# Kernel tuning notes

Hardware: AMD Instinct MI355X
Metric: run time of the kernel (lower is better)

Reference implementation:

```python
import jax, jax.numpy as jnp
import numpy as np

LN_EPS = 1e-5
BN_EPS = 1e-5


def setup_inputs() -> dict:
    key = jax.random.key(0)
    ks = jax.random.split(key, 16)
    b, n = 16, 256
    sc = 0.1
    inp = {
        "x": jax.random.normal(ks[0], (b, n, 4), jnp.float32),
        # proj: Linear(4, 64)
        "proj_w": jax.random.normal(ks[1], (4, 64), jnp.float32) * sc,
        "proj_b": jnp.zeros((64,), jnp.float32),
        # sigma_net: Linear(128,64) -> LayerNorm(64) -> ReLU -> Linear(64,1) -> Softplus
        "s_w1": jax.random.normal(ks[2], (128, 64), jnp.float32) * sc,
        "s_b1": jnp.zeros((64,), jnp.float32),
        "ln_g": jnp.ones((64,), jnp.float32),
        "ln_b": jnp.zeros((64,), jnp.float32),
        "s_w2": jax.random.normal(ks[3], (64, 1), jnp.float32) * sc,
        "s_b2": jnp.zeros((1,), jnp.float32),
        # gnn weight
        "gnn_w": jax.random.normal(ks[4], (64, 64), jnp.float32) * sc,
        # classifier: Linear(128,64) -> BatchNorm1d(64) -> ELU -> Dropout(eval) -> Linear(64,2)
        "c_w1": jax.random.normal(ks[5], (128, 64), jnp.float32) * sc,
        "c_b1": jnp.zeros((64,), jnp.float32),
        "bn_g": jnp.ones((64,), jnp.float32),
        "bn_b": jnp.zeros((64,), jnp.float32),
        "bn_mean": jnp.zeros((64,), jnp.float32),
        "bn_var": jnp.ones((64,), jnp.float32),
        "c_w2": jax.random.normal(ks[6], (64, 2), jnp.float32) * sc,
        "c_b2": jnp.zeros((2,), jnp.float32),
    }
    return inp


def reference(x, proj_w, proj_b, s_w1, s_b1, ln_g, ln_b, s_w2, s_b2,
              gnn_w, c_w1, c_b1, bn_g, bn_b, bn_mean, bn_var, c_w2, c_b2):
    # h: [b, n, 64]
    h = jax.nn.elu(x @ proj_w + proj_b)

    # sigma_net(cat([xi, xj])) == hi @ s_w1[:64] + hj @ s_w1[64:] + s_b1, broadcast pairwise
    a_i = h @ s_w1[:64]            # [b, n, 64]
    a_j = h @ s_w1[64:]            # [b, n, 64]
    pre = a_i[:, :, None, :] + a_j[:, None, :, :] + s_b1  # [b, n, n, 64]
    mu = jnp.mean(pre, axis=-1, keepdims=True)
    var = jnp.mean((pre - mu) ** 2, axis=-1, keepdims=True)
    ln = (pre - mu) * jax.lax.rsqrt(var + LN_EPS) * ln_g + ln_b
    sig_pre = jax.nn.relu(ln) @ s_w2 + s_b2               # [b, n, n, 1]
    sigmas = jax.nn.softplus(sig_pre[..., 0])             # [b, n, n]

    # squared pairwise distance via gram trick: ||hi - hj||^2
    sq = jnp.sum(h * h, axis=-1)                          # [b, n]
    gram = jnp.einsum("bid,bjd->bij", h, h)               # [b, n, n]
    d2 = jnp.maximum(sq[:, :, None] + sq[:, None, :] - 2.0 * gram, 0.0)
    adj = jnp.exp(-d2 / (2.0 * sigmas ** 2 + 1e-6))       # [b, n, n]

    h_agg = jnp.einsum("bij,bjd->bid", adj, h) @ gnn_w    # [b, n, 64]
    h_res = jax.nn.elu(h_agg + h)

    pooled = jnp.concatenate([h_res.mean(axis=1), h_res.max(axis=1)], axis=1)  # [b, 128]

    z = pooled @ c_w1 + c_b1
    z = (z - bn_mean) * jax.lax.rsqrt(bn_var + BN_EPS) * bn_g + bn_b  # BN eval mode
    z = jax.nn.elu(z)                                      # Dropout is identity in eval
    return z @ c_w2 + c_b2                                 # [b, 2]
```

## Files before the change

### kernel.cpp

```cpp
#include <hip/hip_runtime.h>
#include <math.h>

#define OFF_H      0
#define OFF_HT     262144
#define OFF_AI     524288
#define OFF_AJT    786432
#define OFF_SAI    1048576
#define OFF_QAI    1052672
#define OFF_SAJ    1056768
#define OFF_QAJ    1060864
#define OFF_SQH    1064960
#define OFF_HRES   1069056

__device__ __forceinline__ float elu_f(float x) { return x > 0.f ? x : expm1f(x); }

__global__ __launch_bounds__(256) void k1_embed(
    const float* __restrict__ x,
    const float* __restrict__ proj_w, const float* __restrict__ proj_b,
    const float* __restrict__ s_w1, const float* __restrict__ s_b1,
    float* __restrict__ h, float* __restrict__ hT,
    float* __restrict__ a_i, float* __restrict__ a_jT,
    float* __restrict__ sa_i, float* __restrict__ qa_i,
    float* __restrict__ sa_j, float* __restrict__ qa_j,
    float* __restrict__ sqh)
{
    int lane = threadIdx.x & 63;
    int wave = threadIdx.x >> 6;
    int row  = blockIdx.x * 4 + wave;
    int b = row >> 8, i = row & 255;

    __shared__ float hsh[4][64];

    float4 xv = *(const float4*)&x[row*4];
    float hv = xv.x*proj_w[lane] + xv.y*proj_w[64+lane] + xv.z*proj_w[128+lane]
             + xv.w*proj_w[192+lane] + proj_b[lane];
    hv = elu_f(hv);
    hsh[wave][lane] = hv;
    __syncthreads();

    float ai = s_b1[lane], aj = 0.f;
    #pragma unroll 8
    for (int e = 0; e < 64; ++e) {
        float he = hsh[wave][e];
        ai = fmaf(he, s_w1[e*64 + lane], ai);
        aj = fmaf(he, s_w1[(64+e)*64 + lane], aj);
    }
    h[row*64 + lane] = hv;
    hT[b*64*256 + lane*256 + i] = hv;
    a_i[row*64 + lane] = ai;
    a_jT[b*64*256 + lane*256 + i] = aj;

    float v1 = ai, v2 = ai*ai, v3 = aj, v4 = aj*aj, v5 = hv*hv;
    #pragma unroll
    for (int off = 32; off > 0; off >>= 1) {
        v1 += __shfl_xor(v1, off);
        v2 += __shfl_xor(v2, off);
        v3 += __shfl_xor(v3, off);
        v4 += __shfl_xor(v4, off);
        v5 += __shfl_xor(v5, off);
    }
    if (lane == 0) {
        sa_i[row] = v1; qa_i[row] = v2;
        sa_j[row] = v3; qa_j[row] = v4;
        sqh[row]  = v5;
    }
}

#define TI 4
__global__ __launch_bounds__(256) void k2_pair(
    const float* __restrict__ a_i, const float* __restrict__ a_jT,
    const float* __restrict__ h, const float* __restrict__ hT,
    const float* __restrict__ sa_i, const float* __restrict__ qa_i,
    const float* __restrict__ sa_j, const float* __restrict__ qa_j,
    const float* __restrict__ sqh,
    const float* __restrict__ ln_g, const float* __restrict__ ln_b,
    const float* __restrict__ s_w2, const float* __restrict__ s_b2,
    const float* __restrict__ gnn_w,
    float* __restrict__ h_res)
{
    int bi0 = blockIdx.x * TI;
    int b   = bi0 >> 8;
    int j   = threadIdx.x;

    __shared__ float4 aj4[16][256];
    __shared__ float  aiT[64][4], hiT[64][4];
    __shared__ float  gbw[64][4];
    __shared__ float  sai_s[4], qai_s[4], sqi_s[4];
    __shared__ float  adj_sh[256][4];
    __shared__ float  part_sh[4][4][64];
    __shared__ float  hagg_sh[4][64];

    {
        int i = j >> 6, d = j & 63;
        aiT[d][i] = a_i[(bi0+i)*64 + d];
        hiT[d][i] = h[(bi0+i)*64 + d];
    }
    if (j < 64) {
        gbw[j][0] = ln_g[j]; gbw[j][1] = ln_b[j]; gbw[j][2] = s_w2[j]; gbw[j][3] = 0.f;
    }
    if (j < 4) {
        sai_s[j] = sa_i[bi0+j]; qai_s[j] = qa_i[bi0+j]; sqi_s[j] = sqh[bi0+j];
    }
    float saj = sa_j[b*256 + j], qaj = qa_j[b*256 + j], sqj = sqh[b*256 + j];
    float b2  = s_b2[0];
    __syncthreads();

    const float* ajb = a_jT + b*64*256;
    const float* htb = hT   + b*64*256;

    float ga[4] = {0.f,0.f,0.f,0.f}, gh[4] = {0.f,0.f,0.f,0.f};
    #pragma unroll 4
    for (int dg = 0; dg < 16; ++dg) {
        float c[4];
        #pragma unroll
        for (int u = 0; u < 4; ++u) {
            int d = dg*4 + u;
            float ajd = ajb[d*256 + j];
            float hjd = htb[d*256 + j];
            float4 A = *(const float4*)&aiT[d][0];
            float4 H = *(const float4*)&hiT[d][0];
            ga[0] = fmaf(A.x, ajd, ga[0]); ga[1] = fmaf(A.y, ajd, ga[1]);
            ga[2] = fmaf(A.z, ajd, ga[2]); ga[3] = fmaf(A.w, ajd, ga[3]);
            gh[0] = fmaf(H.x, hjd, gh[0]); gh[1] = fmaf(H.y, hjd, gh[1]);
            gh[2] = fmaf(H.z, hjd, gh[2]); gh[3] = fmaf(H.w, hjd, gh[3]);
            c[u] = ajd;
        }
        aj4[dg][j] = make_float4(c[0], c[1], c[2], c[3]);
    }

    float rs4[4], nr4[4], d24[4];
    #pragma unroll
    for (int i = 0; i < 4; ++i) {
        float mu  = (sai_s[i] + saj) * (1.f/64.f);
        float pss = qai_s[i] + qaj + 2.f*ga[i];
        float var = pss * (1.f/64.f) - mu*mu;
        rs4[i] = rsqrtf(var + 1e-5f);
        nr4[i] = -mu * rs4[i];
        d24[i] = fmaxf(sqi_s[i] + sqj - 2.f*gh[i], 0.f);
    }

    float acc[4] = {0.f,0.f,0.f,0.f};
    #pragma unroll 4
    for (int dg = 0; dg < 16; ++dg) {
        float4 ajv = aj4[dg][j];
        float aju[4] = {ajv.x, ajv.y, ajv.z, ajv.w};
        #pragma unroll
        for (int u = 0; u < 4; ++u) {
            int d = dg*4 + u;
            float ajd = aju[u];
            float4 A = *(const float4*)&aiT[d][0];
            float4 G = *(const float4*)&gbw[d][0];
            float t0 = fmaxf(fmaf(fmaf(A.x + ajd, rs4[0], nr4[0]), G.x, G.y), 0.f);
            acc[0] = fmaf(t0, G.z, acc[0]);
            float t1 = fmaxf(fmaf(fmaf(A.y + ajd, rs4[1], nr4[1]), G.x, G.y), 0.f);
            acc[1] = fmaf(t1, G.z, acc[1]);
            float t2 = fmaxf(fmaf(fmaf(A.z + ajd, rs4[2], nr4[2]), G.x, G.y), 0.f);
            acc[2] = fmaf(t2, G.z, acc[2]);
            float t3 = fmaxf(fmaf(fmaf(A.w + ajd, rs4[3], nr4[3]), G.x, G.y), 0.f);
            acc[3] = fmaf(t3, G.z, acc[3]);
        }
    }

    {
        float4 av;
        float sp0 = acc[0] + b2;
        float sg0 = fmaxf(sp0, 0.f) + log1pf(expf(-fabsf(sp0)));
        av.x = expf(-d24[0] / (2.f*sg0*sg0 + 1e-6f));
        float sp1 = acc[1] + b2;
        float sg1 = fmaxf(sp1, 0.f) + log1pf(expf(-fabsf(sp1)));
        av.y = expf(-d24[1] / (2.f*sg1*sg1 + 1e-6f));
        float sp2 = acc[2] + b2;
        float sg2 = fmaxf(sp2, 0.f) + log1pf(expf(-fabsf(sp2)));
        av.z = expf(-d24[2] / (2.f*sg2*sg2 + 1e-6f));
        float sp3 = acc[3] + b2;
        float sg3 = fmaxf(sp3, 0.f) + log1pf(expf(-fabsf(sp3)));
        av.w = expf(-d24[3] / (2.f*sg3*sg3 + 1e-6f));
        *(float4*)&adj_sh[j][0] = av;
    }
    __syncthreads();

    int d = j & 63, q = j >> 6;
    const float* hb = h + b*256*64;
    float part[4] = {0.f,0.f,0.f,0.f};
    #pragma unroll 8
    for (int k = 0; k < 64; ++k) {
        int jj = q*64 + k;
        float hv = hb[jj*64 + d];
        float4 a4 = *(const float4*)&adj_sh[jj][0];
        part[0] = fmaf(a4.x, hv, part[0]);
        part[1] = fmaf(a4.y, hv, part[1]);
        part[2] = fmaf(a4.z, hv, part[2]);
        part[3] = fmaf(a4.w, hv, part[3]);
    }
    #pragma unroll
    for (int i = 0; i < 4; ++i) part_sh[q][i][d] = part[i];
    __syncthreads();

    {
        int i = j >> 6, dd = j & 63;
        hagg_sh[i][dd] = part_sh[0][i][dd] + part_sh[1][i][dd]
                       + part_sh[2][i][dd] + part_sh[3][i][dd];
    }
    __syncthreads();

    {
        int i = j >> 6, lane = j & 63;
        float accg = 0.f;
        #pragma unroll 8
        for (int e = 0; e < 64; ++e)
            accg = fmaf(hagg_sh[i][e], gnn_w[e*64 + lane], accg);
        h_res[(bi0+i)*64 + lane] = elu_f(accg + hiT[lane][i]);
    }
}

__global__ __launch_bounds__(256) void k4_pool_cls(
    const float* __restrict__ h_res,
    const float* __restrict__ c_w1, const float* __restrict__ c_b1,
    const float* __restrict__ bn_g, const float* __restrict__ bn_b,
    const float* __restrict__ bn_mean, const float* __restrict__ bn_var,
    const float* __restrict__ c_w2, const float* __restrict__ c_b2,
    float* __restrict__ out)
{
    int b = blockIdx.x;
    int tid = threadIdx.x;
    int d = tid & 63, q = tid >> 6;
    const float* hb = h_res + b*256*64;

    float sum = 0.f, mx = -INFINITY;
    #pragma unroll 8
    for (int k = 0; k < 64; ++k) {
        float v = hb[(q*64+k)*64 + d];
        sum += v; mx = fmaxf(mx, v);
    }
    __shared__ float sum_sh[256], max_sh[256];
    __shared__ float pm_sh[64], px_sh[64];
    sum_sh[tid] = sum; max_sh[tid] = mx;
    __syncthreads();
    if (tid < 64) {
        float tsum = sum_sh[tid] + sum_sh[64+tid] + sum_sh[128+tid] + sum_sh[192+tid];
        float tmax = fmaxf(fmaxf(max_sh[tid], max_sh[64+tid]),
                           fmaxf(max_sh[128+tid], max_sh[192+tid]));
        pm_sh[tid] = tsum * (1.f/256.f);
        px_sh[tid] = tmax;
    }
    __syncthreads();
    if (tid < 64) {
        float acc = c_b1[tid];
        #pragma unroll
        for (int e = 0; e < 64; ++e) {
            acc += pm_sh[e] * c_w1[e*64 + tid];
            acc += px_sh[e] * c_w1[(64+e)*64 + tid];
        }
        float z = (acc - bn_mean[tid]) * rsqrtf(bn_var[tid] + 1e-5f) * bn_g[tid] + bn_b[tid];
        z = elu_f(z);
        float c0 = z * c_w2[tid*2 + 0];
        float c1 = z * c_w2[tid*2 + 1];
        for (int off = 32; off > 0; off >>= 1) {
            c0 += __shfl_down(c0, off);
            c1 += __shfl_down(c1, off);
        }
        if (tid == 0) {
            out[b*2 + 0] = c0 + c_b2[0];
            out[b*2 + 1] = c1 + c_b2[1];
        }
    }
}

extern "C" void kernel_launch(void* const* d_in, const int* in_sizes, int n_in,
                              void* d_out, int out_size, void* d_ws, size_t ws_size,
                              hipStream_t stream) {
    const float* x       = (const float*)d_in[0];
    const float* proj_w  = (const float*)d_in[1];
    const float* proj_b  = (const float*)d_in[2];
    const float* s_w1    = (const float*)d_in[3];
    const float* s_b1    = (const float*)d_in[4];
    const float* ln_g    = (const float*)d_in[5];
    const float* ln_b    = (const float*)d_in[6];
    const float* s_w2    = (const float*)d_in[7];
    const float* s_b2    = (const float*)d_in[8];
    const float* gnn_w   = (const float*)d_in[9];
    const float* c_w1    = (const float*)d_in[10];
    const float* c_b1    = (const float*)d_in[11];
    const float* bn_g    = (const float*)d_in[12];
    const float* bn_b    = (const float*)d_in[13];
    const float* bn_mean = (const float*)d_in[14];
    const float* bn_var  = (const float*)d_in[15];
    const float* c_w2    = (const float*)d_in[16];
    const float* c_b2    = (const float*)d_in[17];

    float* w = (float*)d_ws;
    float* h     = w + OFF_H;
    float* hT    = w + OFF_HT;
    float* a_i   = w + OFF_AI;
    float* a_jT  = w + OFF_AJT;
    float* sa_i  = w + OFF_SAI;
    float* qa_i  = w + OFF_QAI;
    float* sa_j  = w + OFF_SAJ;
    float* qa_j  = w + OFF_QAJ;
    float* sqh   = w + OFF_SQH;
    float* h_res = w + OFF_HRES;
    float* out   = (float*)d_out;

    k1_embed<<<1024, 256, 0, stream>>>(x, proj_w, proj_b, s_w1, s_b1,
                                       h, hT, a_i, a_jT,
                                       sa_i, qa_i, sa_j, qa_j, sqh);
    k2_pair<<<1024, 256, 0, stream>>>(a_i, a_jT, h, hT,
                                      sa_i, qa_i, sa_j, qa_j, sqh,
                                      ln_g, ln_b, s_w2, s_b2, gnn_w, h_res);
    k4_pool_cls<<<16, 256, 0, stream>>>(h_res, c_w1, c_b1, bn_g, bn_b,
                                        bn_mean, bn_var, c_w2, c_b2, out);
}
```

Baseline: 55.28 us.

## Drop transposed buffers, hold a_j rows in registers, stage s_w1 in LDS

The embed kernel now copies all of s_w1 into shared memory, has each wave process two rows, broadcasts h values with wave shuffles, and no longer writes transposed hT/a_jT. The pair kernel reads each j-row of h and a_j as row-major float4 vectors and keeps a_j in 16 float4 registers instead of a 16 KB shared-memory staging array, with launch bounds requesting 3 blocks per SM. This removes the strided transposed writes and the large LDS buffer, which should allow more blocks per CU. The cost is much higher register pressure, and each thread's row-major loads are 256 bytes apart from its neighbours' rather than coalesced across lanes.

```diff
diff --git a/kernel.cpp b/kernel.cpp
--- a/kernel.cpp
+++ b/kernel.cpp
@@ -2,15 +2,14 @@
 #include <math.h>
 
 #define OFF_H      0
-#define OFF_HT     262144
-#define OFF_AI     524288
-#define OFF_AJT    786432
-#define OFF_SAI    1048576
-#define OFF_QAI    1052672
-#define OFF_SAJ    1056768
-#define OFF_QAJ    1060864
-#define OFF_SQH    1064960
-#define OFF_HRES   1069056
+#define OFF_AI     262144
+#define OFF_AJ     524288
+#define OFF_SAI    786432
+#define OFF_QAI    790528
+#define OFF_SAJ    794624
+#define OFF_QAJ    798720
+#define OFF_SQH    802816
+#define OFF_HRES   806912
 
 __device__ __forceinline__ float elu_f(float x) { return x > 0.f ? x : expm1f(x); }
 
@@ -18,58 +17,62 @@
     const float* __restrict__ x,
     const float* __restrict__ proj_w, const float* __restrict__ proj_b,
     const float* __restrict__ s_w1, const float* __restrict__ s_b1,
-    float* __restrict__ h, float* __restrict__ hT,
-    float* __restrict__ a_i, float* __restrict__ a_jT,
+    float* __restrict__ h, float* __restrict__ a_i, float* __restrict__ a_j,
     float* __restrict__ sa_i, float* __restrict__ qa_i,
     float* __restrict__ sa_j, float* __restrict__ qa_j,
     float* __restrict__ sqh)
 {
-    int lane = threadIdx.x & 63;
-    int wave = threadIdx.x >> 6;
-    int row  = blockIdx.x * 4 + wave;
-    int b = row >> 8, i = row & 255;
-
-    __shared__ float hsh[4][64];
-
-    float4 xv = *(const float4*)&x[row*4];
-    float hv = xv.x*proj_w[lane] + xv.y*proj_w[64+lane] + xv.z*proj_w[128+lane]
-             + xv.w*proj_w[192+lane] + proj_b[lane];
-    hv = elu_f(hv);
-    hsh[wave][lane] = hv;
-    __syncthreads();
-
-    float ai = s_b1[lane], aj = 0.f;
-    #pragma unroll 8
-    for (int e = 0; e < 64; ++e) {
-        float he = hsh[wave][e];
-        ai = fmaf(he, s_w1[e*64 + lane], ai);
-        aj = fmaf(he, s_w1[(64+e)*64 + lane], aj);
-    }
-    h[row*64 + lane] = hv;
-    hT[b*64*256 + lane*256 + i] = hv;
-    a_i[row*64 + lane] = ai;
-    a_jT[b*64*256 + lane*256 + i] = aj;
-
-    float v1 = ai, v2 = ai*ai, v3 = aj, v4 = aj*aj, v5 = hv*hv;
-    #pragma unroll
-    for (int off = 32; off > 0; off >>= 1) {
-        v1 += __shfl_xor(v1, off);
-        v2 += __shfl_xor(v2, off);
-        v3 += __shfl_xor(v3, off);
-        v4 += __shfl_xor(v4, off);
-        v5 += __shfl_xor(v5, off);
-    }
-    if (lane == 0) {
-        sa_i[row] = v1; qa_i[row] = v2;
-        sa_j[row] = v3; qa_j[row] = v4;
-        sqh[row]  = v5;
+    __shared__ float w_sh[8192];
+    int tid = threadIdx.x;
+    #pragma unroll
+    for (int r = 0; r < 8; ++r)
+        *(float4*)&w_sh[(r*256 + tid)*4] = *(const float4*)&s_w1[(r*256 + tid)*4];
+    __syncthreads();
+
+    int lane = tid & 63;
+    int wave = tid >> 6;
+    int row0 = blockIdx.x * 8;
+
+    float pw0 = proj_w[lane], pw1 = proj_w[64+lane], pw2 = proj_w[128+lane],
+          pw3 = proj_w[192+lane], pb = proj_b[lane], b1 = s_b1[lane];
+
+    #pragma unroll
+    for (int r = 0; r < 2; ++r) {
+        int row = row0 + wave*2 + r;
+        float4 xv = *(const float4*)&x[row*4];
+        float hv = elu_f(xv.x*pw0 + xv.y*pw1 + xv.z*pw2 + xv.w*pw3 + pb);
+
+        float ai = b1, aj = 0.f;
+        #pragma unroll 8
+        for (int e = 0; e < 64; ++e) {
+            float he = __shfl(hv, e);
+            ai = fmaf(he, w_sh[e*64 + lane], ai);
+            aj = fmaf(he, w_sh[(64+e)*64 + lane], aj);
+        }
+        h[row*64 + lane]   = hv;
+        a_i[row*64 + lane] = ai;
+        a_j[row*64 + lane] = aj;
+
+        float v1 = ai, v2 = ai*ai, v3 = aj, v4 = aj*aj, v5 = hv*hv;
+        #pragma unroll
+        for (int off = 32; off > 0; off >>= 1) {
+            v1 += __shfl_xor(v1, off);
+            v2 += __shfl_xor(v2, off);
+            v3 += __shfl_xor(v3, off);
+            v4 += __shfl_xor(v4, off);
+            v5 += __shfl_xor(v5, off);
+        }
+        if (lane == 0) {
+            sa_i[row] = v1; qa_i[row] = v2;
+            sa_j[row] = v3; qa_j[row] = v4;
+            sqh[row]  = v5;
+        }
     }
 }
 
-#define TI 4
-__global__ __launch_bounds__(256) void k2_pair(
-    const float* __restrict__ a_i, const float* __restrict__ a_jT,
-    const float* __restrict__ h, const float* __restrict__ hT,
+__global__ __launch_bounds__(256, 3) void k2_pair(
+    const float* __restrict__ a_i, const float* __restrict__ a_jr,
+    const float* __restrict__ h,
     const float* __restrict__ sa_i, const float* __restrict__ qa_i,
     const float* __restrict__ sa_j, const float* __restrict__ qa_j,
     const float* __restrict__ sqh,
@@ -78,17 +81,17 @@
     const float* __restrict__ gnn_w,
     float* __restrict__ h_res)
 {
-    int bi0 = blockIdx.x * TI;
+    int bi0 = blockIdx.x * 4;
     int b   = bi0 >> 8;
     int j   = threadIdx.x;
-
-    __shared__ float4 aj4[16][256];
-    __shared__ float  aiT[64][4], hiT[64][4];
-    __shared__ float  gbw[64][4];
-    __shared__ float  sai_s[4], qai_s[4], sqi_s[4];
-    __shared__ float  adj_sh[256][4];
-    __shared__ float  part_sh[4][4][64];
-    __shared__ float  hagg_sh[4][64];
+    int gj  = b*256 + j;
+
+    __shared__ float aiT[64][4], hiT[64][4];
+    __shared__ float gbw[64][4];
+    __shared__ float sai_s[4], qai_s[4], sqi_s[4];
+    __shared__ float adj_sh[256][4];
+    __shared__ float part_sh[4][4][64];
+    __shared__ float hagg_sh[4][64];
 
     {
         int i = j >> 6, d = j & 63;
@@ -101,31 +104,46 @@
     if (j < 4) {
         sai_s[j] = sa_i[bi0+j]; qai_s[j] = qa_i[bi0+j]; sqi_s[j] = sqh[bi0+j];
     }
-    float saj = sa_j[b*256 + j], qaj = qa_j[b*256 + j], sqj = sqh[b*256 + j];
+    float saj = sa_j[gj], qaj = qa_j[gj], sqj = sqh[gj];
     float b2  = s_b2[0];
     __syncthreads();
 
-    const float* ajb = a_jT + b*64*256;
-    const float* htb = hT   + b*64*256;
-
-    float ga[4] = {0.f,0.f,0.f,0.f}, gh[4] = {0.f,0.f,0.f,0.f};
-    #pragma unroll 4
-    for (int dg = 0; dg < 16; ++dg) {
-        float c[4];
+    float gh[4] = {0.f,0.f,0.f,0.f};
+    {
+        float4 hj[16];
+        const float* hr = h + gj*64;
+        #pragma unroll
+        for (int g = 0; g < 16; ++g) hj[g] = *(const float4*)&hr[g*4];
+        #pragma unroll
+        for (int g = 0; g < 16; ++g) {
+            float c[4] = {hj[g].x, hj[g].y, hj[g].z, hj[g].w};
+            #pragma unroll
+            for (int u = 0; u < 4; ++u) {
+                int d = g*4 + u;
+                float4 Hv = *(const float4*)&hiT[d][0];
+                gh[0] = fmaf(Hv.x, c[u], gh[0]); gh[1] = fmaf(Hv.y, c[u], gh[1]);
+                gh[2] = fmaf(Hv.z, c[u], gh[2]); gh[3] = fmaf(Hv.w, c[u], gh[3]);
+            }
+        }
+    }
+
+    float4 aj[16];
+    {
+        const float* ar = a_jr + gj*64;
+        #pragma unroll
+        for (int g = 0; g < 16; ++g) aj[g] = *(const float4*)&ar[g*4];
+    }
+    float ga[4] = {0.f,0.f,0.f,0.f};
+    #pragma unroll
+    for (int g = 0; g < 16; ++g) {
+        float c[4] = {aj[g].x, aj[g].y, aj[g].z, aj[g].w};
         #pragma unroll
         for (int u = 0; u < 4; ++u) {
-            int d = dg*4 + u;
-            float ajd = ajb[d*256 + j];
-            float hjd = htb[d*256 + j];
+            int d = g*4 + u;
             float4 A = *(const float4*)&aiT[d][0];
-            float4 H = *(const float4*)&hiT[d][0];
-            ga[0] = fmaf(A.x, ajd, ga[0]); ga[1] = fmaf(A.y, ajd, ga[1]);
-            ga[2] = fmaf(A.z, ajd, ga[2]); ga[3] = fmaf(A.w, ajd, ga[3]);
-            gh[0] = fmaf(H.x, hjd, gh[0]); gh[1] = fmaf(H.y, hjd, gh[1]);
-            gh[2] = fmaf(H.z, hjd, gh[2]); gh[3] = fmaf(H.w, hjd, gh[3]);
-            c[u] = ajd;
-        }
-        aj4[dg][j] = make_float4(c[0], c[1], c[2], c[3]);
+            ga[0] = fmaf(A.x, c[u], ga[0]); ga[1] = fmaf(A.y, c[u], ga[1]);
+            ga[2] = fmaf(A.z, c[u], ga[2]); ga[3] = fmaf(A.w, c[u], ga[3]);
+        }
     }
 
     float rs4[4], nr4[4], d24[4];
@@ -140,14 +158,13 @@
     }
 
     float acc[4] = {0.f,0.f,0.f,0.f};
-    #pragma unroll 4
-    for (int dg = 0; dg < 16; ++dg) {
-        float4 ajv = aj4[dg][j];
-        float aju[4] = {ajv.x, ajv.y, ajv.z, ajv.w};
+    #pragma unroll
+    for (int g = 0; g < 16; ++g) {
+        float c[4] = {aj[g].x, aj[g].y, aj[g].z, aj[g].w};
         #pragma unroll
         for (int u = 0; u < 4; ++u) {
-            int d = dg*4 + u;
-            float ajd = aju[u];
+            int d = g*4 + u;
+            float ajd = c[u];
             float4 A = *(const float4*)&aiT[d][0];
             float4 G = *(const float4*)&gbw[d][0];
             float t0 = fmaxf(fmaf(fmaf(A.x + ajd, rs4[0], nr4[0]), G.x, G.y), 0.f);
@@ -290,9 +307,8 @@
 
     float* w = (float*)d_ws;
     float* h     = w + OFF_H;
-    float* hT    = w + OFF_HT;
     float* a_i   = w + OFF_AI;
-    float* a_jT  = w + OFF_AJT;
+    float* a_j   = w + OFF_AJ;
     float* sa_i  = w + OFF_SAI;
     float* qa_i  = w + OFF_QAI;
     float* sa_j  = w + OFF_SAJ;
@@ -301,10 +317,10 @@
     float* h_res = w + OFF_HRES;
     float* out   = (float*)d_out;
 
-    k1_embed<<<1024, 256, 0, stream>>>(x, proj_w, proj_b, s_w1, s_b1,
-                                       h, hT, a_i, a_jT,
-                                       sa_i, qa_i, sa_j, qa_j, sqh);
-    k2_pair<<<1024, 256, 0, stream>>>(a_i, a_jT, h, hT,
+    k1_embed<<<512, 256, 0, stream>>>(x, proj_w, proj_b, s_w1, s_b1,
+                                      h, a_i, a_j,
+                                      sa_i, qa_i, sa_j, qa_j, sqh);
+    k2_pair<<<1024, 256, 0, stream>>>(a_i, a_j, h,
                                       sa_i, qa_i, sa_j, qa_j, sqh,
                                       ln_g, ln_b, s_w2, s_b2, gnn_w, h_res);
     k4_pool_cls<<<16, 256, 0, stream>>>(h_res, c_w1, c_b1, bn_g, bn_b,
```

Result: slower. 132.8 us (+140.2%).
